# Kernel tuning notes

Hardware: AMD Instinct MI355X
Metric: run time of the kernel (lower is better)

## Reference

```python
import jax, jax.numpy as jnp
import numpy as np


def setup_inputs() -> dict:
    key = jax.random.key(0)
    k1, k2, k3 = jax.random.split(key, 3)
    B, S, U = 32, 2048, 1024
    H = jax.random.normal(k1, (B, U), dtype=jnp.float32)
    EO = jax.random.normal(k2, (B, S, U), dtype=jnp.float32)
    W_kernel = jax.random.normal(k3, (U, U), dtype=jnp.float32) * (1.0 / np.sqrt(U))
    W_bias = jnp.zeros((U,), dtype=jnp.float32)
    return {"H": H, "EO": EO, "W_kernel": W_kernel, "W_bias": W_bias}


def reference(H, EO, W_kernel, W_bias):
    # hidden_with_time_axis = expand_dims(H, 1); Dense: H @ W + b -> [B, 1, U]
    proj = (H @ W_kernel + W_bias)[:, None, :]  # [B, 1, U]
    score = proj * EO                            # [B, S, U]
    attention_weights = jax.nn.softmax(score, axis=1)  # softmax over seq axis
    context_vector = jnp.sum(attention_weights * EO, axis=1)  # [B, U]
    return context_vector, attention_weights
```

## Files before the change

kernel.cpp:

```cpp
#include <hip/hip_runtime.h>
#include <math.h>

namespace {
constexpr int kB  = 32;
constexpr int kS  = 2048;
constexpr int kU  = 1024;
constexpr int kUB = 32;
constexpr int kT  = 1024;
constexpr int kSP = kT / 8;
constexpr int kSI = kS / kSP;
constexpr int kW  = kT / 64;

typedef float fvec4 __attribute__((ext_vector_type(4)));

__device__ __forceinline__ unsigned short f2bf(float x) {
    union { float f; unsigned int u; } v; v.f = x;
    unsigned int r = v.u + 0x7fff + ((v.u >> 16) & 1);
    return (unsigned short)(r >> 16);
}
__device__ __forceinline__ float bf2f(unsigned short h) {
    union { float f; unsigned int u; } v; v.u = ((unsigned int)h) << 16;
    return v.f;
}

__global__ void __launch_bounds__(kT, 4)
fused_kernel(const float* __restrict__ EO, const float* __restrict__ H,
             const float* __restrict__ W, const float* __restrict__ bias,
             float* __restrict__ wout, float* __restrict__ ctx_out) {
    __shared__ unsigned short expv[kS][kUB];
    __shared__ float pred[32][kUB];
    __shared__ float projv[kUB];
    __shared__ float partL[kW][8][4];
    __shared__ float partC[kW][8][4];
    __shared__ float rinv_s[kUB];

    const int bx = blockIdx.x;
    const int b  = bx >> 5;
    const int u0 = (bx & 31) * kUB;
    const int t  = threadIdx.x;

    {
        const int uc = t & 31;
        const int kp = t >> 5;
        const float* __restrict__ hrow = H + b * kU + kp * 32;
        const float* __restrict__ wcol = W + (size_t)(kp * 32) * kU + u0 + uc;
        float a = 0.f;
#pragma unroll 8
        for (int k = 0; k < 32; ++k) a = fmaf(hrow[k], wcol[(size_t)k * kU], a);
        pred[kp][uc] = a;
    }
    __syncthreads();
    if (t < kUB) {
        float a = 0.f;
#pragma unroll
        for (int k = 0; k < 32; ++k) a += pred[k][t];
        projv[t] = a + bias[u0 + t];
    }
    __syncthreads();

    const int u4 = t & 7;
    const int sp = t >> 3;
    const int wv = t >> 6;
    const fvec4 p = *(const fvec4*)&projv[u4 * 4];
    const float* __restrict__ ebase = EO + (size_t)b * kS * kU + u0 + u4 * 4;

    float l0 = 0.f, l1 = 0.f, l2 = 0.f, l3 = 0.f;
    float c0 = 0.f, c1 = 0.f, c2 = 0.f, c3 = 0.f;
#pragma unroll
    for (int i = 0; i < kSI; ++i) {
        const int s = sp + kSP * i;
        fvec4 e = *(const fvec4*)(ebase + (size_t)s * kU);
        float e0 = __expf(p.x * e.x), e1 = __expf(p.y * e.y);
        float e2 = __expf(p.z * e.z), e3 = __expf(p.w * e.w);
        l0 += e0; l1 += e1; l2 += e2; l3 += e3;
        c0 = fmaf(e0, e.x, c0); c1 = fmaf(e1, e.y, c1);
        c2 = fmaf(e2, e.z, c2); c3 = fmaf(e3, e.w, c3);
        ushort4 pk = {f2bf(e0), f2bf(e1), f2bf(e2), f2bf(e3)};
        *(ushort4*)&expv[s][u4 * 4] = pk;
    }

#pragma unroll
    for (int m = 8; m <= 32; m <<= 1) {
        l0 += __shfl_xor(l0, m); l1 += __shfl_xor(l1, m);
        l2 += __shfl_xor(l2, m); l3 += __shfl_xor(l3, m);
        c0 += __shfl_xor(c0, m); c1 += __shfl_xor(c1, m);
        c2 += __shfl_xor(c2, m); c3 += __shfl_xor(c3, m);
    }
    if ((t & 63) < 8) {
        partL[wv][u4][0] = l0; partL[wv][u4][1] = l1;
        partL[wv][u4][2] = l2; partL[wv][u4][3] = l3;
        partC[wv][u4][0] = c0; partC[wv][u4][1] = c1;
        partC[wv][u4][2] = c2; partC[wv][u4][3] = c3;
    }
    __syncthreads();
    if (t < kUB) {
        const int g = t >> 2, j = t & 3;
        float L = 0.f, C = 0.f;
#pragma unroll
        for (int w = 0; w < kW; ++w) { L += partL[w][g][j]; C += partC[w][g][j]; }
        const float r = 1.f / L;
        rinv_s[t] = r;
        ctx_out[(size_t)b * kU + u0 + t] = C * r;
    }
    __syncthreads();

    const fvec4 r4 = *(const fvec4*)&rinv_s[u4 * 4];
    float* __restrict__ wbase = wout + (size_t)b * kS * kU + u0 + u4 * 4;
#pragma unroll
    for (int i = 0; i < kSI; ++i) {
        const int s = sp + kSP * i;
        ushort4 pk = *(const ushort4*)&expv[s][u4 * 4];
        fvec4 w;
        w.x = bf2f(pk.x) * r4.x; w.y = bf2f(pk.y) * r4.y;
        w.z = bf2f(pk.z) * r4.z; w.w = bf2f(pk.w) * r4.w;
        __builtin_nontemporal_store(w, (fvec4*)(wbase + (size_t)s * kU));
    }
}
}

extern "C" void kernel_launch(void* const* d_in, const int* in_sizes, int n_in,
                              void* d_out, int out_size, void* d_ws, size_t ws_size,
                              hipStream_t stream) {
    const float* H    = (const float*)d_in[0];
    const float* EO   = (const float*)d_in[1];
    const float* W    = (const float*)d_in[2];
    const float* bias = (const float*)d_in[3];

    float* ctx_out = (float*)d_out;
    float* w_out   = (float*)d_out + (size_t)kB * kU;

    fused_kernel<<<dim3(kB * (kU / kUB)), kT, 0, stream>>>(EO, H, W, bias, w_out, ctx_out);
}
```

Before: 97.96 us.

## Make kernel persistent and overlap previous tile's weight stores with next tile's loads

Launches one block per CU (256 blocks), each handling four (batch, unit-slice) tiles in sequence. Inside the sequence loop, the attention-weight stores for the previous tile are interleaved with the EO loads and exp computation for the current tile, so reads and writes overlap. Before, each large-LDS block finished its load phase before starting its store phase. The projection step is reorganised to compute all four tiles' projections up front with longer per-thread dot products. The cost is more register pressure and serial per-block work, so tail imbalance and latency hiding now depend on a single block per CU.

```diff
diff --git a/kernel.cpp b/kernel.cpp
--- a/kernel.cpp
+++ b/kernel.cpp
@@ -7,9 +7,11 @@
 constexpr int kU  = 1024;
 constexpr int kUB = 32;
 constexpr int kT  = 1024;
-constexpr int kSP = kT / 8;
+constexpr int kSP = 128;
 constexpr int kSI = kS / kSP;
 constexpr int kW  = kT / 64;
+constexpr int kGrid  = 256;
+constexpr int kTiles = (kB * (kU / kUB)) / kGrid;
 
 typedef float fvec4 __attribute__((ext_vector_type(4)));
 
@@ -28,92 +30,113 @@
              const float* __restrict__ W, const float* __restrict__ bias,
              float* __restrict__ wout, float* __restrict__ ctx_out) {
     __shared__ unsigned short expv[kS][kUB];
-    __shared__ float pred[32][kUB];
-    __shared__ float projv[kUB];
+    __shared__ float pred[8][128];
+    __shared__ float projv[kTiles][kUB];
     __shared__ float partL[kW][8][4];
     __shared__ float partC[kW][8][4];
     __shared__ float rinv_s[kUB];
 
-    const int bx = blockIdx.x;
-    const int b  = bx >> 5;
-    const int u0 = (bx & 31) * kUB;
+    const int c  = blockIdx.x;
     const int t  = threadIdx.x;
+    const int u4 = t & 7;
+    const int sp = t >> 3;
+    const int wv = t >> 6;
 
     {
-        const int uc = t & 31;
-        const int kp = t >> 5;
-        const float* __restrict__ hrow = H + b * kU + kp * 32;
-        const float* __restrict__ wcol = W + (size_t)(kp * 32) * kU + u0 + uc;
+        const int pair = t & 127;
+        const int kp   = t >> 7;
+        const int tj   = pair >> 5;
+        const int uc   = pair & 31;
+        const int wk   = tj * kGrid + c;
+        const int b    = wk >> 5;
+        const int u0   = (wk & 31) * kUB;
+        const float* __restrict__ hrow = H + b * kU + kp * 128;
+        const float* __restrict__ wcol = W + (size_t)(kp * 128) * kU + u0 + uc;
         float a = 0.f;
 #pragma unroll 8
-        for (int k = 0; k < 32; ++k) a = fmaf(hrow[k], wcol[(size_t)k * kU], a);
-        pred[kp][uc] = a;
+        for (int k = 0; k < 128; ++k) a = fmaf(hrow[k], wcol[(size_t)k * kU], a);
+        pred[kp][pair] = a;
     }
     __syncthreads();
-    if (t < kUB) {
+    if (t < 128) {
+        const int tj = t >> 5, uc = t & 31;
         float a = 0.f;
 #pragma unroll
-        for (int k = 0; k < 32; ++k) a += pred[k][t];
-        projv[t] = a + bias[u0 + t];
+        for (int k = 0; k < 8; ++k) a += pred[k][t];
+        const int wk = tj * kGrid + c;
+        projv[tj][uc] = a + bias[(wk & 31) * kUB + uc];
     }
     __syncthreads();
 
-    const int u4 = t & 7;
-    const int sp = t >> 3;
-    const int wv = t >> 6;
-    const fvec4 p = *(const fvec4*)&projv[u4 * 4];
-    const float* __restrict__ ebase = EO + (size_t)b * kS * kU + u0 + u4 * 4;
+    float* wbase_prev = nullptr;
+    fvec4  r4_prev = {0.f, 0.f, 0.f, 0.f};
 
-    float l0 = 0.f, l1 = 0.f, l2 = 0.f, l3 = 0.f;
-    float c0 = 0.f, c1 = 0.f, c2 = 0.f, c3 = 0.f;
 #pragma unroll
-    for (int i = 0; i < kSI; ++i) {
-        const int s = sp + kSP * i;
-        fvec4 e = *(const fvec4*)(ebase + (size_t)s * kU);
-        float e0 = __expf(p.x * e.x), e1 = __expf(p.y * e.y);
-        float e2 = __expf(p.z * e.z), e3 = __expf(p.w * e.w);
-        l0 += e0; l1 += e1; l2 += e2; l3 += e3;
-        c0 = fmaf(e0, e.x, c0); c1 = fmaf(e1, e.y, c1);
-        c2 = fmaf(e2, e.z, c2); c3 = fmaf(e3, e.w, c3);
-        ushort4 pk = {f2bf(e0), f2bf(e1), f2bf(e2), f2bf(e3)};
-        *(ushort4*)&expv[s][u4 * 4] = pk;
+    for (int tj = 0; tj < kTiles; ++tj) {
+        const int wk = tj * kGrid + c;
+        const int b  = wk >> 5;
+        const int u0 = (wk & 31) * kUB;
+        const fvec4 p = *(const fvec4*)&projv[tj][u4 * 4];
+        const float* __restrict__ ebase = EO + (size_t)b * kS * kU + u0 + u4 * 4;
+
+        float l0 = 0.f, l1 = 0.f, l2 = 0.f, l3 = 0.f;
+        float c0 = 0.f, c1 = 0.f, c2 = 0.f, c3 = 0.f;
+#pragma unroll
+        for (int i = 0; i < kSI; ++i) {
+            const int s = sp + kSP * i;
+            fvec4 e = *(const fvec4*)(ebase + (size_t)s * kU);
+            if (tj > 0) {
+                ushort4 pk = *(const ushort4*)&expv[s][u4 * 4];
+                fvec4 w;
+                w.x = bf2f(pk.x) * r4_prev.x; w.y = bf2f(pk.y) * r4_prev.y;
+                w.z = bf2f(pk.z) * r4_prev.z; w.w = bf2f(pk.w) * r4_prev.w;
+                __builtin_nontemporal_store(w, (fvec4*)(wbase_prev + (size_t)s * kU));
+            }
+            float e0 = __expf(p.x * e.x), e1 = __expf(p.y * e.y);
+            float e2 = __expf(p.z * e.z), e3 = __expf(p.w * e.w);
+            l0 += e0; l1 += e1; l2 += e2; l3 += e3;
+            c0 = fmaf(e0, e.x, c0); c1 = fmaf(e1, e.y, c1);
+            c2 = fmaf(e2, e.z, c2); c3 = fmaf(e3, e.w, c3);
+            ushort4 pk = {f2bf(e0), f2bf(e1), f2bf(e2), f2bf(e3)};
+            *(ushort4*)&expv[s][u4 * 4] = pk;
+        }
+
+#pragma unroll
+        for (int m = 8; m <= 32; m <<= 1) {
+            l0 += __shfl_xor(l0, m); l1 += __shfl_xor(l1, m);
+            l2 += __shfl_xor(l2, m); l3 += __shfl_xor(l3, m);
+            c0 += __shfl_xor(c0, m); c1 += __shfl_xor(c1, m);
+            c2 += __shfl_xor(c2, m); c3 += __shfl_xor(c3, m);
+        }
+        if ((t & 63) < 8) {
+            partL[wv][u4][0] = l0; partL[wv][u4][1] = l1;
+            partL[wv][u4][2] = l2; partL[wv][u4][3] = l3;
+            partC[wv][u4][0] = c0; partC[wv][u4][1] = c1;
+            partC[wv][u4][2] = c2; partC[wv][u4][3] = c3;
+        }
+        __syncthreads();
+        if (t < kUB) {
+            const int g = t >> 2, j = t & 3;
+            float L = 0.f, C = 0.f;
+#pragma unroll
+            for (int w = 0; w < kW; ++w) { L += partL[w][g][j]; C += partC[w][g][j]; }
+            const float r = 1.f / L;
+            rinv_s[t] = r;
+            ctx_out[(size_t)b * kU + u0 + t] = C * r;
+        }
+        __syncthreads();
+        r4_prev = *(const fvec4*)&rinv_s[u4 * 4];
+        wbase_prev = wout + (size_t)b * kS * kU + u0 + u4 * 4;
     }
 
-#pragma unroll
-    for (int m = 8; m <= 32; m <<= 1) {
-        l0 += __shfl_xor(l0, m); l1 += __shfl_xor(l1, m);
-        l2 += __shfl_xor(l2, m); l3 += __shfl_xor(l3, m);
-        c0 += __shfl_xor(c0, m); c1 += __shfl_xor(c1, m);
-        c2 += __shfl_xor(c2, m); c3 += __shfl_xor(c3, m);
-    }
-    if ((t & 63) < 8) {
-        partL[wv][u4][0] = l0; partL[wv][u4][1] = l1;
-        partL[wv][u4][2] = l2; partL[wv][u4][3] = l3;
-        partC[wv][u4][0] = c0; partC[wv][u4][1] = c1;
-        partC[wv][u4][2] = c2; partC[wv][u4][3] = c3;
-    }
-    __syncthreads();
-    if (t < kUB) {
-        const int g = t >> 2, j = t & 3;
-        float L = 0.f, C = 0.f;
-#pragma unroll
-        for (int w = 0; w < kW; ++w) { L += partL[w][g][j]; C += partC[w][g][j]; }
-        const float r = 1.f / L;
-        rinv_s[t] = r;
-        ctx_out[(size_t)b * kU + u0 + t] = C * r;
-    }
-    __syncthreads();
-
-    const fvec4 r4 = *(const fvec4*)&rinv_s[u4 * 4];
-    float* __restrict__ wbase = wout + (size_t)b * kS * kU + u0 + u4 * 4;
 #pragma unroll
     for (int i = 0; i < kSI; ++i) {
         const int s = sp + kSP * i;
         ushort4 pk = *(const ushort4*)&expv[s][u4 * 4];
         fvec4 w;
-        w.x = bf2f(pk.x) * r4.x; w.y = bf2f(pk.y) * r4.y;
-        w.z = bf2f(pk.z) * r4.z; w.w = bf2f(pk.w) * r4.w;
-        __builtin_nontemporal_store(w, (fvec4*)(wbase + (size_t)s * kU));
+        w.x = bf2f(pk.x) * r4_prev.x; w.y = bf2f(pk.y) * r4_prev.y;
+        w.z = bf2f(pk.z) * r4_prev.z; w.w = bf2f(pk.w) * r4_prev.w;
+        __builtin_nontemporal_store(w, (fvec4*)(wbase_prev + (size_t)s * kU));
     }
 }
 }
@@ -129,5 +152,5 @@
     float* ctx_out = (float*)d_out;
     float* w_out   = (float*)d_out + (size_t)kB * kU;
 
-    fused_kernel<<<dim3(kB * (kU / kUB)), kT, 0, stream>>>(EO, H, W, bias, w_out, ctx_out);
+    fused_kernel<<<dim3(kGrid), kT, 0, stream>>>(EO, H, W, bias, w_out, ctx_out);
 }
```

New measurement: 143.9 us. 1.47x slower.
